# Kernel tuning notes

Measured on AMD Instinct MI355X. Metric: run time of the kernel, lower is better.

## Reference

```python
import jax, jax.numpy as jnp
import numpy as np

HIDDEN = 2048
NUM_HEADS = 16
HEAD_DIM = HIDDEN // NUM_HEADS


def setup_inputs() -> dict:
    key = jax.random.key(0)
    ks = jax.random.split(key, 5)
    B, S, H = 2, 2048, HIDDEN
    # xavier_uniform bounds
    qkv_bound = float(np.sqrt(6.0 / (H + 3 * H)))
    out_bound = float(np.sqrt(6.0 / (H + H)))
    return {
        "x": jax.random.normal(ks[0], (B, S, H), dtype=jnp.float32),
        "W_qkv": jax.random.uniform(ks[1], (3 * H, H), minval=-qkv_bound, maxval=qkv_bound, dtype=jnp.float32),
        "b_qkv": jnp.zeros((3 * H,), dtype=jnp.float32),
        "W_out": jax.random.uniform(ks[2], (H, H), minval=-out_bound, maxval=out_bound, dtype=jnp.float32),
        "b_out": jnp.zeros((H,), dtype=jnp.float32),
    }


def reference(x, W_qkv, b_qkv, W_out, b_out):
    B, S, H = x.shape
    # fused QKV projection (torch Linear: x @ W.T + b)
    qkv = x @ W_qkv.T + b_qkv                      # (B, S, 3H)
    q, k, v = jnp.split(qkv, 3, axis=-1)
    # (B, S, H) -> (B, N, S, D)
    def to_heads(t):
        return t.reshape(B, S, NUM_HEADS, HEAD_DIM).transpose(0, 2, 1, 3)
    q, k, v = to_heads(q), to_heads(k), to_heads(v)
    scale = HEAD_DIM ** -0.5
    scores = jnp.einsum("bnqd,bnkd->bnqk", q, k) * scale  # (B, N, S, S)
    causal = jnp.triu(jnp.ones((S, S), dtype=bool), k=1)
    scores = jnp.where(causal, -jnp.inf, scores)
    attn = jax.nn.softmax(scores, axis=-1)
    out = jnp.einsum("bnqk,bnkd->bnqd", attn, v)           # (B, N, S, D)
    out = out.transpose(0, 2, 1, 3).reshape(B, S, H)
    return out @ W_out.T + b_out
```

## Files before the change

kernel.cpp:

```cpp
#include <hip/hip_runtime.h>
#include <stdint.h>


using bf16x8 = __attribute__((ext_vector_type(8))) __bf16;
using f32x4  = __attribute__((ext_vector_type(4))) float;

#define S_LEN 2048
#define HID   2048
#define NHEAD 16
#define DHEAD 128
#define QSCALE_L2E (0.08838834764831845f * 1.4426950408889634f)

__device__ __forceinline__ unsigned short f2bf(float f) {
  union { float f; unsigned int u; } c; c.f = f;
  unsigned int u = c.u;
  return (unsigned short)((u + 0x7FFFu + ((u >> 16) & 1u)) >> 16);
}

__device__ __forceinline__ unsigned int pkbf(float a, float b) {
  union { __bf16 h[2]; unsigned int u; } x;
  x.h[0] = (__bf16)a; x.h[1] = (__bf16)b;
  return x.u;
}

__device__ __forceinline__ void gload_lds16(const void* g, void* l) {
  __builtin_amdgcn_global_load_lds(
      (const __attribute__((address_space(1))) unsigned int*)g,
      (__attribute__((address_space(3))) unsigned int*)l, 16, 0, 0);
}

__device__ __forceinline__ f32x4 mfma16(bf16x8 a, bf16x8 b, f32x4 c) {
  return __builtin_amdgcn_mfma_f32_16x16x32_bf16(a, b, c, 0, 0, 0);
}

__device__ __forceinline__ float hmax4(f32x4 v) {
  return fmaxf(fmaxf(v[0], v[1]), fmaxf(v[2], v[3]));
}

__global__ void cvt_bf16(const float* __restrict__ in, unsigned short* __restrict__ out, int n) {
  const int n4 = n >> 2;
  const int stride = gridDim.x * blockDim.x;
  for (int i = blockIdx.x * blockDim.x + threadIdx.x; i < n4; i += stride) {
    float4 v = reinterpret_cast<const float4*>(in)[i];
    ushort4 o;
    o.x = f2bf(v.x); o.y = f2bf(v.y); o.z = f2bf(v.z); o.w = f2bf(v.w);
    reinterpret_cast<ushort4*>(out)[i] = o;
  }
}

template<int EPI>
__global__ __launch_bounds__(256) void gemm_bt(
    const unsigned short* __restrict__ A, const unsigned short* __restrict__ Bw,
    const float* __restrict__ bias, int K, int N,
    unsigned short* __restrict__ q_out, unsigned short* __restrict__ k_out,
    unsigned short* __restrict__ vt_out, float* __restrict__ c_out)
{
  __shared__ char lsA[128 * 128];
  __shared__ char lsB[128 * 128];
  const int tid = threadIdx.x;
  const int l = tid & 63, w = tid >> 6;
  const int wr = w >> 1, wc = w & 1;
  const int bm = blockIdx.x * 128, bn = blockIdx.y * 128;
  const int row16 = l & 15, kg = l >> 4;

  f32x4 acc[4][4] = {};

  for (int k0 = 0; k0 < K; k0 += 64) {
    #pragma unroll
    for (int c = 0; c < 4; ++c) {
      const int o = c * 4096 + tid * 16;
      const int r = o >> 7;
      const int cb = (o & 127) ^ ((r & 7) << 4);
      gload_lds16((const char*)A + ((size_t)(bm + r) * K + k0) * 2 + cb,
                  lsA + c * 4096 + (w << 10));
      gload_lds16((const char*)Bw + ((size_t)(bn + r) * K + k0) * 2 + cb,
                  lsB + c * 4096 + (w << 10));
    }
    __syncthreads();

    #pragma unroll
    for (int h = 0; h < 2; ++h) {
      bf16x8 af[4], bfr[4];
      #pragma unroll
      for (int i = 0; i < 4; ++i) {
        const int ra = wr * 64 + i * 16 + row16;
        af[i]  = *(const bf16x8*)(lsA + ra * 128 + ((h * 64 + kg * 16) ^ ((ra & 7) << 4)));
        const int rb = wc * 64 + i * 16 + row16;
        bfr[i] = *(const bf16x8*)(lsB + rb * 128 + ((h * 64 + kg * 16) ^ ((rb & 7) << 4)));
      }
      #pragma unroll
      for (int i = 0; i < 4; ++i)
        #pragma unroll
        for (int j = 0; j < 4; ++j)
          acc[i][j] = mfma16(af[i], bfr[j], acc[i][j]);
    }
    __syncthreads();
  }

  const int r0 = kg * 4;
  #pragma unroll
  for (int i = 0; i < 4; ++i) {
    const int row = bm + wr * 64 + i * 16 + r0;
    #pragma unroll
    for (int j = 0; j < 4; ++j) {
      const int col = bn + wc * 64 + j * 16 + row16;
      const float bv = bias[col];
      if (EPI == 1) {
        #pragma unroll
        for (int r = 0; r < 4; ++r)
          c_out[(size_t)(row + r) * N + col] = acc[i][j][r] + bv;
      } else {
        const int sec = col >> 11;
        const int within = col & 2047;
        const int head = within >> 7, d = within & 127;
        #pragma unroll
        for (int r = 0; r < 4; ++r) {
          const int rr = row + r;
          const int b = rr >> 11, s = rr & 2047;
          const int bh = b * NHEAD + head;
          const float v = acc[i][j][r] + bv;
          if (sec == 0)
            q_out[((size_t)bh * S_LEN + s) * DHEAD + d] = f2bf(v * QSCALE_L2E);
          else if (sec == 1)
            k_out[((size_t)bh * S_LEN + s) * DHEAD + d] = f2bf(v);
          else
            vt_out[((size_t)bh * DHEAD + d) * S_LEN + s] = f2bf(v);
        }
      }
    }
  }
}

__global__ __launch_bounds__(256, 2) void attn_fwd(
    const unsigned short* __restrict__ Q, const unsigned short* __restrict__ Kk,
    const unsigned short* __restrict__ Vt, unsigned short* __restrict__ O)
{
  __shared__ char lsK[2][64 * 256];
  __shared__ char lsV[2][128 * 128];
  __shared__ char lsP[4][32 * 128];
  const int tid = threadIdx.x, l = tid & 63, w = tid >> 6;
  const int row16 = l & 15, kg = l >> 4;
  const int qb = (blockIdx.y < 16) ? (15 - (int)blockIdx.x) : (int)blockIdx.x;
  const int bh = blockIdx.y;
  const int bidx = bh >> 4, head = bh & 15;

  const char* Qh = (const char*)(Q  + (size_t)bh * S_LEN * DHEAD);
  const char* Kh = (const char*)(Kk + (size_t)bh * S_LEN * DHEAD);
  const char* Vh = (const char*)(Vt + (size_t)bh * DHEAD * S_LEN);

  const int q0w = qb * 128 + w * 32;

  bf16x8 qf[2][4];
  #pragma unroll
  for (int qs = 0; qs < 2; ++qs)
    #pragma unroll
    for (int t = 0; t < 4; ++t)
      qf[qs][t] = *(const bf16x8*)(Qh + ((size_t)(q0w + qs * 16 + row16) * DHEAD + t * 32 + kg * 8) * 2);

  float m[2]  = {-1e30f, -1e30f};
  float ls[2] = {0.f, 0.f};
  f32x4 oacc[2][8] = {};

  const int last = 2 * qb + 1;

#define STAGE(buf, kt_) do {                                                     \
    _Pragma("unroll")                                                            \
    for (int c = 0; c < 4; ++c) {                                                \
      const int o = c * 4096 + tid * 16;                                         \
      const int rk = o >> 8, cbk = (o & 255) ^ ((rk & 7) << 4);                  \
      gload_lds16(Kh + (size_t)((kt_) * 64 + rk) * 256 + cbk,                    \
                  lsK[buf] + c * 4096 + (w << 10));                              \
      const int dv = o >> 7, cbv = (o & 127) ^ ((dv & 7) << 4);                  \
      gload_lds16(Vh + (size_t)dv * 4096 + (size_t)(kt_) * 128 + cbv,            \
                  lsV[buf] + c * 4096 + (w << 10));                              \
    } } while (0)

  STAGE(0, 0);
  __syncthreads();

  int cur = 0;
  for (int kt = 0; ; ++kt) {
    if (kt < last) STAGE(cur ^ 1, kt + 1);

    if (kt * 64 <= q0w + 31) {
      const char* Kc = lsK[cur];
      const char* Vc = lsV[cur];
      char* Pl = lsP[w];

      f32x4 sc[4][2] = {};
      #pragma unroll
      for (int j = 0; j < 4; ++j) {
        const int krow = j * 16 + row16;
        const int sw = (krow & 7) << 4;
        bf16x8 kf[4];
        #pragma unroll
        for (int t = 0; t < 4; ++t)
          kf[t] = *(const bf16x8*)(Kc + krow * 256 + ((t * 64 + kg * 16) ^ sw));
        #pragma unroll
        for (int t = 0; t < 4; ++t) {
          sc[j][0] = mfma16(kf[t], qf[0][t], sc[j][0]);
          sc[j][1] = mfma16(kf[t], qf[1][t], sc[j][1]);
        }
      }

      if (kt >= 2 * qb) {
        #pragma unroll
        for (int j = 0; j < 4; ++j) {
          const int kvb = kt * 64 + j * 16 + kg * 4;
          #pragma unroll
          for (int qs = 0; qs < 2; ++qs) {
            const int qq = q0w + qs * 16 + row16;
            #pragma unroll
            for (int r = 0; r < 4; ++r)
              if (kvb + r > qq) sc[j][qs][r] = -1e30f;
          }
        }
      }

      float pm[2], al[2] = {1.f, 1.f};
      #pragma unroll
      for (int qs = 0; qs < 2; ++qs) {
        float mx = fmaxf(fmaxf(hmax4(sc[0][qs]), hmax4(sc[1][qs])),
                         fmaxf(hmax4(sc[2][qs]), hmax4(sc[3][qs])));
        mx = fmaxf(mx, __shfl_xor(mx, 16, 64));
        mx = fmaxf(mx, __shfl_xor(mx, 32, 64));
        pm[qs] = mx;
      }
      const bool need = (pm[0] > m[0] + 8.f) || (pm[1] > m[1] + 8.f);
      if (__any(need)) {
        const float n0 = fmaxf(m[0], pm[0]), n1 = fmaxf(m[1], pm[1]);
        al[0] = exp2f(m[0] - n0); al[1] = exp2f(m[1] - n1);
        m[0] = n0; m[1] = n1;
        float aq[2][4];
        #pragma unroll
        for (int qs2 = 0; qs2 < 2; ++qs2)
          #pragma unroll
          for (int r = 0; r < 4; ++r)
            aq[qs2][r] = __shfl(al[qs2], kg * 4 + r, 64);
        #pragma unroll
        for (int qs2 = 0; qs2 < 2; ++qs2)
          #pragma unroll
          for (int dt = 0; dt < 8; ++dt)
            #pragma unroll
            for (int r = 0; r < 4; ++r)
              oacc[qs2][dt][r] *= aq[qs2][r];
      }

      #pragma unroll
      for (int qs = 0; qs < 2; ++qs) {
        const int q = qs * 16 + row16;
        const int psw = (q & 7) << 4;
        float ps = 0.f;
        #pragma unroll
        for (int j = 0; j < 4; ++j) {
          const float p0 = exp2f(sc[j][qs][0] - m[qs]);
          const float p1 = exp2f(sc[j][qs][1] - m[qs]);
          const float p2 = exp2f(sc[j][qs][2] - m[qs]);
          const float p3 = exp2f(sc[j][qs][3] - m[qs]);
          ps += (p0 + p1) + (p2 + p3);
          uint2 pw; pw.x = pkbf(p0, p1); pw.y = pkbf(p2, p3);
          *(uint2*)(Pl + q * 128 + ((j * 32 + kg * 8) ^ psw)) = pw;
        }
        ps += __shfl_xor(ps, 16, 64);
        ps += __shfl_xor(ps, 32, 64);
        ls[qs] = ls[qs] * al[qs] + ps;
      }

      bf16x8 pa[2][2];
      #pragma unroll
      for (int qs2 = 0; qs2 < 2; ++qs2) {
        const int q = qs2 * 16 + row16;
        #pragma unroll
        for (int ks = 0; ks < 2; ++ks)
          pa[qs2][ks] = *(const bf16x8*)(Pl + q * 128 + ((ks * 64 + kg * 16) ^ ((q & 7) << 4)));
      }
      #pragma unroll
      for (int dt = 0; dt < 8; ++dt) {
        const int drow = dt * 16 + row16;
        const int vsw = (drow & 7) << 4;
        bf16x8 v0 = *(const bf16x8*)(Vc + drow * 128 + ((kg * 16) ^ vsw));
        bf16x8 v1 = *(const bf16x8*)(Vc + drow * 128 + ((64 + kg * 16) ^ vsw));
        oacc[0][dt] = mfma16(pa[0][0], v0, oacc[0][dt]);
        oacc[0][dt] = mfma16(pa[0][1], v1, oacc[0][dt]);
        oacc[1][dt] = mfma16(pa[1][0], v0, oacc[1][dt]);
        oacc[1][dt] = mfma16(pa[1][1], v1, oacc[1][dt]);
      }
    }

    __syncthreads();
    if (kt == last) break;
    cur ^= 1;
  }
#undef STAGE

  #pragma unroll
  for (int qs2 = 0; qs2 < 2; ++qs2) {
    #pragma unroll
    for (int r = 0; r < 4; ++r) {
      const float lr = __shfl(ls[qs2], kg * 4 + r, 64);
      const float inv = 1.0f / lr;
      const int q = q0w + qs2 * 16 + kg * 4 + r;
      const size_t orow = (size_t)(bidx * S_LEN + q) * HID + (size_t)head * DHEAD;
      #pragma unroll
      for (int dt = 0; dt < 8; ++dt)
        O[orow + dt * 16 + row16] = f2bf(oacc[qs2][dt][r] * inv);
    }
  }
}

extern "C" void kernel_launch(void* const* d_in, const int* in_sizes, int n_in,
                              void* d_out, int out_size, void* d_ws, size_t ws_size,
                              hipStream_t stream) {
  const float* x    = (const float*)d_in[0];
  const float* Wqkv = (const float*)d_in[1];
  const float* bqkv = (const float*)d_in[2];
  const float* Wout = (const float*)d_in[3];
  const float* bout = (const float*)d_in[4];
  float* out = (float*)d_out;

  if (ws_size < 100663296) return;
  char* ws = (char*)d_ws;
  unsigned short* Qb    = (unsigned short*)(ws);
  unsigned short* Kb    = (unsigned short*)(ws + 16777216);
  unsigned short* Vtb   = (unsigned short*)(ws + 2 * 16777216);
  unsigned short* xb    = (unsigned short*)(ws + 3 * 16777216);
  unsigned short* Ob    = xb;
  unsigned short* Wqkvb = (unsigned short*)(ws + 4 * 16777216);
  unsigned short* Woutb = (unsigned short*)(ws + 4 * 16777216 + 25165824);

  cvt_bf16<<<2048, 256, 0, stream>>>(x,    xb,    4096 * 2048);
  cvt_bf16<<<2048, 256, 0, stream>>>(Wqkv, Wqkvb, 6144 * 2048);
  cvt_bf16<<<1024, 256, 0, stream>>>(Wout, Woutb, 2048 * 2048);

  gemm_bt<0><<<dim3(32, 48), 256, 0, stream>>>(xb, Wqkvb, bqkv, 2048, 6144,
                                               Qb, Kb, Vtb, nullptr);
  attn_fwd<<<dim3(16, 32), 256, 0, stream>>>(Qb, Kb, Vtb, Ob);
  gemm_bt<1><<<dim3(32, 16), 256, 0, stream>>>(Ob, Woutb, bout, 2048, 2048,
                                               nullptr, nullptr, nullptr, out);
}
```

Measured before the change: 284.3 us.

## Replace GEMM with triple-buffered 512-thread kernel using larger tiles and block swizzle

The old 128x128 single-buffered GEMM kernel is replaced with a templated kernel that uses 256x256 or 128x256 tiles and 512 threads. It keeps a three-slot LDS ring of K=32 chunks, issuing async global-to-LDS loads two chunks ahead and waiting with explicit vmcnt counters. It also adds a blockIdx swizzle for L2 locality, a different LDS swizzle layout, and s_setprio around the MFMA block. The aim is to overlap memory loads with MFMA work and raise data reuse per tile, at the cost of more LDS and registers per block and reliance on hand-tuned waitcnt correctness.

```diff
diff --git a/kernel.cpp b/kernel.cpp
--- a/kernel.cpp
+++ b/kernel.cpp
@@ -9,6 +9,7 @@
 #define HID   2048
 #define NHEAD 16
 #define DHEAD 128
+#define KDIM  2048
 #define QSCALE_L2E (0.08838834764831845f * 1.4426950408889634f)
 
 __device__ __forceinline__ unsigned short f2bf(float f) {
@@ -35,6 +36,12 @@
 
 __device__ __forceinline__ float hmax4(f32x4 v) {
   return fmaxf(fmaxf(v[0], v[1]), fmaxf(v[2], v[3]));
+}
+
+template<int N> __device__ __forceinline__ void waitvm() {
+  if constexpr (N == 3)      asm volatile("s_waitcnt vmcnt(3)" ::: "memory");
+  else if constexpr (N == 4) asm volatile("s_waitcnt vmcnt(4)" ::: "memory");
+  else                       asm volatile("s_waitcnt vmcnt(0)" ::: "memory");
 }
 
 __global__ void cvt_bf16(const float* __restrict__ in, unsigned short* __restrict__ out, int n) {
@@ -48,62 +55,117 @@
   }
 }
 
-template<int EPI>
-__global__ __launch_bounds__(256) void gemm_bt(
+template<int BM, int BN, int EPI>
+__global__ __launch_bounds__(512, 2) void gemm_p3(
     const unsigned short* __restrict__ A, const unsigned short* __restrict__ Bw,
-    const float* __restrict__ bias, int K, int N,
+    const float* __restrict__ bias, int N,
     unsigned short* __restrict__ q_out, unsigned short* __restrict__ k_out,
     unsigned short* __restrict__ vt_out, float* __restrict__ c_out)
 {
-  __shared__ char lsA[128 * 128];
-  __shared__ char lsB[128 * 128];
-  const int tid = threadIdx.x;
-  const int l = tid & 63, w = tid >> 6;
-  const int wr = w >> 1, wc = w & 1;
-  const int bm = blockIdx.x * 128, bn = blockIdx.y * 128;
+  constexpr int KB2   = 2 * KDIM;
+  constexpr int NCH   = KDIM / 32;
+  constexpr int ABYT  = BM * 64;
+  constexpr int BBYT  = BN * 64;
+  constexpr int LPA   = BM / 128;
+  constexpr int LPB   = BN / 128;
+  constexpr int LPC   = LPA + LPB;
+  constexpr int M_SUB = BM / 32;
+  constexpr int N_SUB = BN / 64;
+  constexpr int MBC   = 4096 / BM;
+
+  __shared__ char lsA[3 * ABYT];
+  __shared__ char lsB[3 * BBYT];
+
+  const int tid = threadIdx.x, l = tid & 63, w = tid >> 6;
+  const int wr = w >> 2, wc = w & 3;
   const int row16 = l & 15, kg = l >> 4;
 
-  f32x4 acc[4][4] = {};
-
-  for (int k0 = 0; k0 < K; k0 += 64) {
-    #pragma unroll
-    for (int c = 0; c < 4; ++c) {
-      const int o = c * 4096 + tid * 16;
-      const int r = o >> 7;
-      const int cb = (o & 127) ^ ((r & 7) << 4);
-      gload_lds16((const char*)A + ((size_t)(bm + r) * K + k0) * 2 + cb,
-                  lsA + c * 4096 + (w << 10));
-      gload_lds16((const char*)Bw + ((size_t)(bn + r) * K + k0) * 2 + cb,
-                  lsB + c * 4096 + (w << 10));
+  const int nwg = gridDim.x;
+  const int bid = blockIdx.x;
+  const int swz = (bid & 7) * (nwg >> 3) + (bid >> 3);
+  const int bm = (swz % MBC) * BM, bn = (swz / MBC) * BN;
+
+  const char* Ag = (const char*)A + (size_t)bm * KB2;
+  const char* Bg = (const char*)Bw + (size_t)bn * KB2;
+
+  f32x4 acc[M_SUB][N_SUB] = {};
+
+#define STAGE(cc, sl) do {                                                     \
+    _Pragma("unroll")                                                          \
+    for (int p = 0; p < LPA; ++p) {                                            \
+      const int ob = (p * 8 + w) << 10;                                        \
+      const int o = ob + l * 16;                                               \
+      const int m2 = o >> 7, sw = o & 127;                                     \
+      const int t = sw ^ (((m2 << 1) & 7) << 4);                               \
+      const int odd = (t >> 6) & 1;                                            \
+      const int m = (m2 << 1) | odd;                                           \
+      const int kb = (t ^ (odd << 4)) & 63;                                    \
+      gload_lds16(Ag + (size_t)m * KB2 + (cc) * 64 + kb,                       \
+                  lsA + (sl) * ABYT + ob);                                     \
+    }                                                                          \
+    _Pragma("unroll")                                                          \
+    for (int p = 0; p < LPB; ++p) {                                            \
+      const int ob = (p * 8 + w) << 10;                                        \
+      const int o = ob + l * 16;                                               \
+      const int m2 = o >> 7, sw = o & 127;                                     \
+      const int t = sw ^ (((m2 << 1) & 7) << 4);                               \
+      const int odd = (t >> 6) & 1;                                            \
+      const int m = (m2 << 1) | odd;                                           \
+      const int kb = (t ^ (odd << 4)) & 63;                                    \
+      gload_lds16(Bg + (size_t)m * KB2 + (cc) * 64 + kb,                       \
+                  lsB + (sl) * BBYT + ob);                                     \
+    } } while (0)
+
+  STAGE(0, 0);
+  STAGE(1, 1);
+  waitvm<LPC>();
+  asm volatile("s_barrier" ::: "memory");
+
+  int sl = 0;
+  for (int c = 0; c < NCH; ++c) {
+    int cs = c + 2; if (cs >= NCH) cs -= NCH;
+    int s2 = sl + 2; if (s2 >= 3) s2 -= 3;
+    STAGE(cs, s2);
+
+    const char* Ac = lsA + sl * ABYT;
+    const char* Bc = lsB + sl * BBYT;
+    bf16x8 af[M_SUB], bf[N_SUB];
+    #pragma unroll
+    for (int i = 0; i < M_SUB; ++i) {
+      const int m = wr * (BM / 2) + i * 16 + row16;
+      af[i] = *(const bf16x8*)(Ac + (m >> 1) * 128 +
+              ((((m & 1) << 6) | (kg << 4)) ^ ((m & 7) << 4)));
     }
-    __syncthreads();
-
-    #pragma unroll
-    for (int h = 0; h < 2; ++h) {
-      bf16x8 af[4], bfr[4];
-      #pragma unroll
-      for (int i = 0; i < 4; ++i) {
-        const int ra = wr * 64 + i * 16 + row16;
-        af[i]  = *(const bf16x8*)(lsA + ra * 128 + ((h * 64 + kg * 16) ^ ((ra & 7) << 4)));
-        const int rb = wc * 64 + i * 16 + row16;
-        bfr[i] = *(const bf16x8*)(lsB + rb * 128 + ((h * 64 + kg * 16) ^ ((rb & 7) << 4)));
-      }
-      #pragma unroll
-      for (int i = 0; i < 4; ++i)
-        #pragma unroll
-        for (int j = 0; j < 4; ++j)
-          acc[i][j] = mfma16(af[i], bfr[j], acc[i][j]);
+    #pragma unroll
+    for (int j = 0; j < N_SUB; ++j) {
+      const int n = wc * (BN / 4) + j * 16 + row16;
+      bf[j] = *(const bf16x8*)(Bc + (n >> 1) * 128 +
+              ((((n & 1) << 6) | (kg << 4)) ^ ((n & 7) << 4)));
     }
-    __syncthreads();
+
+    __builtin_amdgcn_s_setprio(1);
+    #pragma unroll
+    for (int i = 0; i < M_SUB; ++i)
+      #pragma unroll
+      for (int j = 0; j < N_SUB; ++j)
+        acc[i][j] = mfma16(af[i], bf[j], acc[i][j]);
+    __builtin_amdgcn_s_setprio(0);
+
+    waitvm<LPC>();
+    __builtin_amdgcn_sched_barrier(0);
+    asm volatile("s_barrier" ::: "memory");
+
+    sl = sl + 1; if (sl == 3) sl = 0;
   }
-
-  const int r0 = kg * 4;
+#undef STAGE
+  waitvm<0>();
+
   #pragma unroll
-  for (int i = 0; i < 4; ++i) {
-    const int row = bm + wr * 64 + i * 16 + r0;
-    #pragma unroll
-    for (int j = 0; j < 4; ++j) {
-      const int col = bn + wc * 64 + j * 16 + row16;
+  for (int i = 0; i < M_SUB; ++i) {
+    const int row = bm + wr * (BM / 2) + i * 16 + kg * 4;
+    #pragma unroll
+    for (int j = 0; j < N_SUB; ++j) {
+      const int col = bn + wc * (BN / 4) + j * 16 + row16;
       const float bv = bias[col];
       if (EPI == 1) {
         #pragma unroll
@@ -332,9 +394,9 @@
   cvt_bf16<<<2048, 256, 0, stream>>>(Wqkv, Wqkvb, 6144 * 2048);
   cvt_bf16<<<1024, 256, 0, stream>>>(Wout, Woutb, 2048 * 2048);
 
-  gemm_bt<0><<<dim3(32, 48), 256, 0, stream>>>(xb, Wqkvb, bqkv, 2048, 6144,
-                                               Qb, Kb, Vtb, nullptr);
+  gemm_p3<256, 256, 0><<<384, 512, 0, stream>>>(xb, Wqkvb, bqkv, 6144,
+                                                Qb, Kb, Vtb, nullptr);
   attn_fwd<<<dim3(16, 32), 256, 0, stream>>>(Qb, Kb, Vtb, Ob);
-  gemm_bt<1><<<dim3(32, 16), 256, 0, stream>>>(Ob, Woutb, bout, 2048, 2048,
-                                               nullptr, nullptr, nullptr, out);
-}
+  gemm_p3<128, 256, 1><<<256, 512, 0, stream>>>(Ob, Woutb, bout, 2048,
+                                                nullptr, nullptr, nullptr, out);
+}
```

Result: slower. 385.8 us (+35.7%).

## Replace QKV GEMM with 256x256-tile, 8-wave, double-buffered pipelined kernel

Applied to the files above, without the earlier changes.

Swaps the QKV projection GEMM for a dedicated kernel using 256x256 output tiles, 512 threads and double-buffered LDS. Global-to-LDS loads for the next K chunk are interleaved with MFMA phases using explicit barriers, waitcnts and setprio, and block IDs are swizzled for L2 reuse. This aims to hide memory latency and raise data reuse per tile. The cost is 128KB of LDS per block and fragile hand-written synchronisation; the output GEMM is split out as its own non-templated kernel with the same behaviour.

```diff
diff --git a/kernel.cpp b/kernel.cpp
--- a/kernel.cpp
+++ b/kernel.cpp
@@ -9,6 +9,7 @@
 #define HID   2048
 #define NHEAD 16
 #define DHEAD 128
+#define KDIM  2048
 #define QSCALE_L2E (0.08838834764831845f * 1.4426950408889634f)
 
 __device__ __forceinline__ unsigned short f2bf(float f) {
@@ -48,13 +49,169 @@
   }
 }
 
-template<int EPI>
-__global__ __launch_bounds__(256) void gemm_bt(
+__global__ __launch_bounds__(512, 2) void gemm_qkv8(
     const unsigned short* __restrict__ A, const unsigned short* __restrict__ Bw,
-    const float* __restrict__ bias, int K, int N,
+    const float* __restrict__ bias,
     unsigned short* __restrict__ q_out, unsigned short* __restrict__ k_out,
-    unsigned short* __restrict__ vt_out, float* __restrict__ c_out)
+    unsigned short* __restrict__ vt_out)
 {
+  __shared__ char lsA[2][32768];
+  __shared__ char lsB[2][32768];
+  const int tid = threadIdx.x, l = tid & 63, w = tid >> 6;
+  const int wr = w >> 2, wc = w & 3;
+  const int row16 = l & 15, kg = l >> 4;
+
+  const int bid = blockIdx.x;
+  const int swz = (bid & 7) * 48 + (bid >> 3);
+  const int bm = (swz & 15) * 256, bn = (swz >> 4) * 256;
+  const char* Ag = (const char*)A + (size_t)bm * (KDIM * 2);
+  const char* Bg = (const char*)Bw + (size_t)bn * (KDIM * 2);
+
+  f32x4 acc[8][4] = {};
+
+  float bv[4];
+  #pragma unroll
+  for (int j = 0; j < 4; ++j) bv[j] = bias[bn + wc * 64 + j * 16 + row16];
+  asm volatile("" :: "v"(bv[0]), "v"(bv[1]), "v"(bv[2]), "v"(bv[3]));
+
+#define BAR   asm volatile("s_barrier" ::: "memory")
+#define LGKM0 asm volatile("s_waitcnt lgkmcnt(0)" ::: "memory"); __builtin_amdgcn_sched_barrier(0)
+#define VM4   asm volatile("s_waitcnt vmcnt(4)" ::: "memory")
+#define PRIO1 __builtin_amdgcn_s_setprio(1)
+#define PRIO0 __builtin_amdgcn_s_setprio(0)
+
+#define STAGE_A(buf, k0, qa) do {                                              \
+    _Pragma("unroll")                                                          \
+    for (int p = 0; p < 2; ++p) {                                              \
+      const int o = tid * 16;                                                  \
+      const int r = p * 128 + (qa) * 64 + (o >> 7);                            \
+      const int cb = (o & 127) ^ ((r & 7) << 4);                               \
+      gload_lds16(Ag + (size_t)r * (KDIM * 2) + (k0) * 2 + cb,                 \
+                  lsA[buf] + p * 16384 + (qa) * 8192 + o);                     \
+    } } while (0)
+
+#define STAGE_B(buf, k0, qb) do {                                              \
+    _Pragma("unroll")                                                          \
+    for (int p = 0; p < 2; ++p) {                                              \
+      const int o = tid * 16;                                                  \
+      const int blk = o >> 12;                                                 \
+      const int r = p * 128 + blk * 64 + (qb) * 32 + ((o >> 7) & 31);          \
+      const int cb = (o & 127) ^ ((r & 7) << 4);                               \
+      gload_lds16(Bg + (size_t)r * (KDIM * 2) + (k0) * 2 + cb,                 \
+                  lsB[buf] + p * 16384 + blk * 8192 + (qb) * 4096 + (o & 4095)); \
+    } } while (0)
+
+#define RD_A(dst, i0) do { _Pragma("unroll")                                   \
+    for (int i = 0; i < 4; ++i) {                                              \
+      const int m = wr * 128 + ((i0) + i) * 16 + row16;                        \
+      _Pragma("unroll")                                                        \
+      for (int h = 0; h < 2; ++h)                                              \
+        dst[i][h] = *(const bf16x8*)(Ac + m * 128 + ((h * 64 + kg * 16) ^ ((m & 7) << 4))); \
+    } } while (0)
+
+#define RD_B(dst, j0) do { _Pragma("unroll")                                   \
+    for (int j = 0; j < 2; ++j) {                                              \
+      const int n = wc * 64 + ((j0) + j) * 16 + row16;                         \
+      _Pragma("unroll")                                                        \
+      for (int h = 0; h < 2; ++h)                                              \
+        dst[j][h] = *(const bf16x8*)(Bc + n * 128 + ((h * 64 + kg * 16) ^ ((n & 7) << 4))); \
+    } } while (0)
+
+#define MM(afrag, bfrag, i0, j0) do { _Pragma("unroll")                        \
+    for (int i = 0; i < 4; ++i) { _Pragma("unroll")                            \
+      for (int j = 0; j < 2; ++j) { _Pragma("unroll")                          \
+        for (int h = 0; h < 2; ++h)                                            \
+          acc[(i0) + i][(j0) + j] = mfma16(afrag[i][h], bfrag[j][h], acc[(i0) + i][(j0) + j]); \
+    } } } while (0)
+
+  STAGE_A(0, 0, 0); STAGE_B(0, 0, 0); STAGE_A(0, 0, 1); STAGE_B(0, 0, 1);
+  asm volatile("s_waitcnt vmcnt(0)" ::: "memory");
+  BAR;
+
+  bf16x8 afl[4][2], afh[4][2], bfl[2][2], bfh[2][2];
+  constexpr int NCH = KDIM / 64;
+
+  #pragma unroll 1
+  for (int t = 0; t < NCH - 1; ++t) {
+    const int cur = t & 1, nxt = cur ^ 1;
+    const char* Ac = lsA[cur];
+    const char* Bc = lsB[cur];
+    const int k1 = (t + 1) * 64;
+    RD_A(afl, 0); RD_B(bfl, 0);
+    STAGE_A(nxt, k1, 0);
+    BAR; LGKM0;
+    PRIO1; MM(afl, bfl, 0, 0); PRIO0;
+    VM4; BAR;
+    RD_A(afh, 4);
+    STAGE_B(nxt, k1, 0);
+    BAR; LGKM0;
+    PRIO1; MM(afh, bfl, 4, 0); PRIO0;
+    VM4; BAR;
+    RD_B(bfh, 2);
+    STAGE_A(nxt, k1, 1);
+    BAR; LGKM0;
+    PRIO1; MM(afl, bfh, 0, 2); PRIO0;
+    BAR;
+    STAGE_B(nxt, k1, 1);
+    BAR;
+    PRIO1; MM(afh, bfh, 4, 2); PRIO0;
+    VM4; BAR;
+  }
+  {
+    const char* Ac = lsA[(NCH - 1) & 1];
+    const char* Bc = lsB[(NCH - 1) & 1];
+    RD_A(afl, 0); RD_B(bfl, 0);
+    MM(afl, bfl, 0, 0);
+    asm volatile("s_waitcnt vmcnt(2)" ::: "memory");
+    RD_A(afh, 4);
+    MM(afh, bfl, 4, 0);
+    asm volatile("s_waitcnt vmcnt(0)" ::: "memory");
+    RD_B(bfh, 2);
+    MM(afl, bfh, 0, 2);
+    MM(afh, bfh, 4, 2);
+  }
+#undef STAGE_A
+#undef STAGE_B
+#undef RD_A
+#undef RD_B
+#undef MM
+#undef BAR
+#undef LGKM0
+#undef VM4
+#undef PRIO1
+#undef PRIO0
+
+  #pragma unroll
+  for (int i = 0; i < 8; ++i) {
+    const int row = bm + wr * 128 + i * 16 + kg * 4;
+    #pragma unroll
+    for (int j = 0; j < 4; ++j) {
+      const int col = bn + wc * 64 + j * 16 + row16;
+      const int sec = col >> 11;
+      const int within = col & 2047;
+      const int head = within >> 7, d = within & 127;
+      #pragma unroll
+      for (int r = 0; r < 4; ++r) {
+        const int rr = row + r;
+        const int b = rr >> 11, s = rr & 2047;
+        const int bh = b * NHEAD + head;
+        const float v = acc[i][j][r] + bv[j];
+        if (sec == 0)
+          q_out[((size_t)bh * S_LEN + s) * DHEAD + d] = f2bf(v * QSCALE_L2E);
+        else if (sec == 1)
+          k_out[((size_t)bh * S_LEN + s) * DHEAD + d] = f2bf(v);
+        else
+          vt_out[((size_t)bh * DHEAD + d) * S_LEN + s] = f2bf(v);
+      }
+    }
+  }
+}
+
+__global__ __launch_bounds__(256) void gemm_out(
+    const unsigned short* __restrict__ A, const unsigned short* __restrict__ Bw,
+    const float* __restrict__ bias, float* __restrict__ c_out)
+{
+  constexpr int K = KDIM, N = HID;
   __shared__ char lsA[128 * 128];
   __shared__ char lsB[128 * 128];
   const int tid = threadIdx.x;
@@ -97,36 +254,16 @@
     __syncthreads();
   }
 
-  const int r0 = kg * 4;
   #pragma unroll
   for (int i = 0; i < 4; ++i) {
-    const int row = bm + wr * 64 + i * 16 + r0;
+    const int row = bm + wr * 64 + i * 16 + kg * 4;
     #pragma unroll
     for (int j = 0; j < 4; ++j) {
       const int col = bn + wc * 64 + j * 16 + row16;
-      const float bv = bias[col];
-      if (EPI == 1) {
-        #pragma unroll
-        for (int r = 0; r < 4; ++r)
-          c_out[(size_t)(row + r) * N + col] = acc[i][j][r] + bv;
-      } else {
-        const int sec = col >> 11;
-        const int within = col & 2047;
-        const int head = within >> 7, d = within & 127;
-        #pragma unroll
-        for (int r = 0; r < 4; ++r) {
-          const int rr = row + r;
-          const int b = rr >> 11, s = rr & 2047;
-          const int bh = b * NHEAD + head;
-          const float v = acc[i][j][r] + bv;
-          if (sec == 0)
-            q_out[((size_t)bh * S_LEN + s) * DHEAD + d] = f2bf(v * QSCALE_L2E);
-          else if (sec == 1)
-            k_out[((size_t)bh * S_LEN + s) * DHEAD + d] = f2bf(v);
-          else
-            vt_out[((size_t)bh * DHEAD + d) * S_LEN + s] = f2bf(v);
-        }
-      }
+      const float bvj = bias[col];
+      #pragma unroll
+      for (int r = 0; r < 4; ++r)
+        c_out[(size_t)(row + r) * N + col] = acc[i][j][r] + bvj;
     }
   }
 }
@@ -332,9 +469,7 @@
   cvt_bf16<<<2048, 256, 0, stream>>>(Wqkv, Wqkvb, 6144 * 2048);
   cvt_bf16<<<1024, 256, 0, stream>>>(Wout, Woutb, 2048 * 2048);
 
-  gemm_bt<0><<<dim3(32, 48), 256, 0, stream>>>(xb, Wqkvb, bqkv, 2048, 6144,
-                                               Qb, Kb, Vtb, nullptr);
+  gemm_qkv8<<<384, 512, 0, stream>>>(xb, Wqkvb, bqkv, Qb, Kb, Vtb);
   attn_fwd<<<dim3(16, 32), 256, 0, stream>>>(Qb, Kb, Vtb, Ob);
-  gemm_bt<1><<<dim3(32, 16), 256, 0, stream>>>(Ob, Woutb, bout, 2048, 2048,
-                                               nullptr, nullptr, nullptr, out);
-}
+  gemm_out<<<dim3(32, 16), 256, 0, stream>>>(Ob, Woutb, bout, out);
+}
```

New measurement: 317.4 us. 11.6% more time.

## Replace generic GEMM with multi-stage pipelined 512-thread QKV and output GEMMs

Applied to the files above, without the earlier changes.

Splits the templated GEMM into two specialized kernels. The QKV GEMM uses 256x384 tiles with a 3-stage LDS ring, and the output GEMM uses 128x256 tiles with a 4-stage ring. Both use 512 threads, K-step 64, explicit vmcnt waits, raw s_barrier and MFMA priority boosting, and a swizzled block order for L2 reuse. The aim is to overlap global loads with MFMA work and cut per-iteration sync overhead, at the cost of larger LDS use, more registers and a single wave of 256 blocks with hardcoded sizes.

```diff
diff --git a/kernel.cpp b/kernel.cpp
--- a/kernel.cpp
+++ b/kernel.cpp
@@ -9,6 +9,7 @@
 #define HID   2048
 #define NHEAD 16
 #define DHEAD 128
+#define KDIM  2048
 #define QSCALE_L2E (0.08838834764831845f * 1.4426950408889634f)
 
 __device__ __forceinline__ unsigned short f2bf(float f) {
@@ -48,85 +49,225 @@
   }
 }
 
-template<int EPI>
-__global__ __launch_bounds__(256) void gemm_bt(
+#define BAR   asm volatile("s_barrier" ::: "memory")
+#define VM(n) asm volatile("s_waitcnt vmcnt(" #n ")" ::: "memory")
+#define PRIO1 __builtin_amdgcn_s_setprio(1)
+#define PRIO0 __builtin_amdgcn_s_setprio(0)
+
+
+__global__ __launch_bounds__(512) void gemm_qkv(
     const unsigned short* __restrict__ A, const unsigned short* __restrict__ Bw,
-    const float* __restrict__ bias, int K, int N,
+    const float* __restrict__ bias,
     unsigned short* __restrict__ q_out, unsigned short* __restrict__ k_out,
-    unsigned short* __restrict__ vt_out, float* __restrict__ c_out)
+    unsigned short* __restrict__ vt_out)
 {
-  __shared__ char lsA[128 * 128];
-  __shared__ char lsB[128 * 128];
-  const int tid = threadIdx.x;
-  const int l = tid & 63, w = tid >> 6;
-  const int wr = w >> 1, wc = w & 1;
-  const int bm = blockIdx.x * 128, bn = blockIdx.y * 128;
+  constexpr int ABYT = 256 * 64;
+  constexpr int BBYT = 384 * 64;
+  __shared__ char lsA[3 * ABYT];
+  __shared__ char lsB[3 * BBYT];
+
+  const int tid = threadIdx.x, l = tid & 63, w = tid >> 6;
+  const int wr = w >> 2, wc = w & 3;
   const int row16 = l & 15, kg = l >> 4;
 
+  const int bid = blockIdx.x;
+  const int swz = (bid & 7) * 32 + (bid >> 3);
+  const int bm = (swz & 15) * 256, bn = (swz >> 4) * 384;
+  const char* Ag = (const char*)A + (size_t)bm * (KDIM * 2);
+  const char* Bg = (const char*)Bw + (size_t)bn * (KDIM * 2);
+
+  f32x4 acc[8][6] = {};
+
+#define STAGE_A(cc, dstb) do { _Pragma("unroll")                               \
+    for (int p = 0; p < 2; ++p) {                                              \
+      const int o = p * 8192 + tid * 16;                                       \
+      const int r = o >> 6, c = o & 63;                                        \
+      gload_lds16(Ag + (size_t)r * (KDIM * 2) + (cc) * 64 +                    \
+                  (c ^ (((r >> 1) & 3) << 4)),                                 \
+                  (dstb) + p * 8192 + (w << 10));                              \
+    } } while (0)
+
+#define STAGE_B(cc, dstb) do { _Pragma("unroll")                               \
+    for (int p = 0; p < 3; ++p) {                                              \
+      const int o = p * 8192 + tid * 16;                                       \
+      const int r = o >> 6, c = o & 63;                                        \
+      gload_lds16(Bg + (size_t)r * (KDIM * 2) + (cc) * 64 +                    \
+                  (c ^ (((r >> 1) & 3) << 4)),                                 \
+                  (dstb) + p * 8192 + (w << 10));                              \
+    } } while (0)
+
+  STAGE_A(0, lsA); STAGE_B(0, lsB);
+  STAGE_A(1, lsA + ABYT); STAGE_B(1, lsB + BBYT);
+  VM(5);
+  BAR;
+
+  int sl = 0;
+  #pragma unroll 1
+  for (int t = 0; t < 64; ++t) {
+    const int s2 = (sl == 0) ? 2 : sl - 1;
+    const char* Ac = lsA + sl * ABYT;
+    const char* Bc = lsB + sl * BBYT;
+    char* A2 = lsA + s2 * ABYT;
+    char* B2 = lsB + s2 * BBYT;
+
+    bf16x8 af[8], bl[3], bh[3];
+    if (t < 62) STAGE_A(t + 2, A2);
+    #pragma unroll
+    for (int i = 0; i < 8; ++i) {
+      const int m = wr * 128 + i * 16 + row16;
+      af[i] = *(const bf16x8*)(Ac + m * 64 + ((kg * 16) ^ (((m >> 1) & 3) << 4)));
+    }
+    #pragma unroll
+    for (int j = 0; j < 3; ++j) {
+      const int n = wc * 96 + j * 16 + row16;
+      bl[j] = *(const bf16x8*)(Bc + n * 64 + ((kg * 16) ^ (((n >> 1) & 3) << 4)));
+    }
+    PRIO1;
+    #pragma unroll
+    for (int i = 0; i < 8; ++i)
+      #pragma unroll
+      for (int j = 0; j < 3; ++j)
+        acc[i][j] = mfma16(af[i], bl[j], acc[i][j]);
+    PRIO0;
+    BAR;
+
+    if (t < 62) STAGE_B(t + 2, B2);
+    #pragma unroll
+    for (int j = 0; j < 3; ++j) {
+      const int n = wc * 96 + (j + 3) * 16 + row16;
+      bh[j] = *(const bf16x8*)(Bc + n * 64 + ((kg * 16) ^ (((n >> 1) & 3) << 4)));
+    }
+    PRIO1;
+    #pragma unroll
+    for (int i = 0; i < 8; ++i)
+      #pragma unroll
+      for (int j = 0; j < 3; ++j)
+        acc[i][j + 3] = mfma16(af[i], bh[j], acc[i][j + 3]);
+    PRIO0;
+    if (t < 62)      VM(5);
+    else if (t == 62) VM(0);
+    BAR;
+
+    sl = (sl == 2) ? 0 : sl + 1;
+  }
+#undef STAGE_A
+#undef STAGE_B
+
+  #pragma unroll
+  for (int j = 0; j < 6; ++j) {
+    const int col = bn + wc * 96 + j * 16 + row16;
+    const float bvj = bias[col];
+    const int sec = col >> 11;
+    const int within = col & 2047;
+    const int head = within >> 7, d = within & 127;
+    #pragma unroll
+    for (int i = 0; i < 8; ++i) {
+      const int row = bm + wr * 128 + i * 16 + kg * 4;
+      #pragma unroll
+      for (int r = 0; r < 4; ++r) {
+        const int rr = row + r;
+        const int b = rr >> 11, s = rr & 2047;
+        const int bh2 = b * NHEAD + head;
+        const float v = acc[i][j][r] + bvj;
+        if (sec == 0)
+          q_out[((size_t)bh2 * S_LEN + s) * DHEAD + d] = f2bf(v * QSCALE_L2E);
+        else if (sec == 1)
+          k_out[((size_t)bh2 * S_LEN + s) * DHEAD + d] = f2bf(v);
+        else
+          vt_out[((size_t)bh2 * DHEAD + d) * S_LEN + s] = f2bf(v);
+      }
+    }
+  }
+}
+
+__global__ __launch_bounds__(512) void gemm_out(
+    const unsigned short* __restrict__ A, const unsigned short* __restrict__ Bw,
+    const float* __restrict__ bias, float* __restrict__ c_out)
+{
+  constexpr int ABYT = 128 * 64;
+  constexpr int BBYT = 256 * 64;
+  __shared__ char lsA[4 * ABYT];
+  __shared__ char lsB[4 * BBYT];
+
+  const int tid = threadIdx.x, l = tid & 63, w = tid >> 6;
+  const int wr = w >> 2, wc = w & 3;
+  const int row16 = l & 15, kg = l >> 4;
+
+  const int bid = blockIdx.x;
+  const int swz = (bid & 7) * 32 + (bid >> 3);
+  const int bm = (swz & 31) * 128, bn = (swz >> 5) * 256;
+  const char* Ag = (const char*)A + (size_t)bm * (KDIM * 2);
+  const char* Bg = (const char*)Bw + (size_t)bn * (KDIM * 2);
+
   f32x4 acc[4][4] = {};
 
-  for (int k0 = 0; k0 < K; k0 += 64) {
-    #pragma unroll
-    for (int c = 0; c < 4; ++c) {
-      const int o = c * 4096 + tid * 16;
-      const int r = o >> 7;
-      const int cb = (o & 127) ^ ((r & 7) << 4);
-      gload_lds16((const char*)A + ((size_t)(bm + r) * K + k0) * 2 + cb,
-                  lsA + c * 4096 + (w << 10));
-      gload_lds16((const char*)Bw + ((size_t)(bn + r) * K + k0) * 2 + cb,
-                  lsB + c * 4096 + (w << 10));
-    }
-    __syncthreads();
-
-    #pragma unroll
-    for (int h = 0; h < 2; ++h) {
-      bf16x8 af[4], bfr[4];
-      #pragma unroll
-      for (int i = 0; i < 4; ++i) {
-        const int ra = wr * 64 + i * 16 + row16;
-        af[i]  = *(const bf16x8*)(lsA + ra * 128 + ((h * 64 + kg * 16) ^ ((ra & 7) << 4)));
-        const int rb = wc * 64 + i * 16 + row16;
-        bfr[i] = *(const bf16x8*)(lsB + rb * 128 + ((h * 64 + kg * 16) ^ ((rb & 7) << 4)));
-      }
-      #pragma unroll
-      for (int i = 0; i < 4; ++i)
-        #pragma unroll
-        for (int j = 0; j < 4; ++j)
-          acc[i][j] = mfma16(af[i], bfr[j], acc[i][j]);
-    }
-    __syncthreads();
-  }
-
-  const int r0 = kg * 4;
+#define STAGE_A(cc, dstb) do {                                                 \
+    const int o = tid * 16;                                                    \
+    const int r = o >> 6, c = o & 63;                                          \
+    gload_lds16(Ag + (size_t)r * (KDIM * 2) + (cc) * 64 +                      \
+                (c ^ (((r >> 1) & 3) << 4)),                                   \
+                (dstb) + (w << 10));                                           \
+  } while (0)
+
+#define STAGE_B(cc, dstb) do { _Pragma("unroll")                               \
+    for (int p = 0; p < 2; ++p) {                                              \
+      const int o = p * 8192 + tid * 16;                                       \
+      const int r = o >> 6, c = o & 63;                                        \
+      gload_lds16(Bg + (size_t)r * (KDIM * 2) + (cc) * 64 +                    \
+                  (c ^ (((r >> 1) & 3) << 4)),                                 \
+                  (dstb) + p * 8192 + (w << 10));                              \
+    } } while (0)
+
+  STAGE_A(0, lsA);              STAGE_B(0, lsB);
+  STAGE_A(1, lsA + ABYT);       STAGE_B(1, lsB + BBYT);
+  STAGE_A(2, lsA + 2 * ABYT);   STAGE_B(2, lsB + 2 * BBYT);
+  VM(6);
+  BAR;
+
+  #pragma unroll 1
+  for (int t = 0; t < 64; ++t) {
+    const int sl = t & 3, s3 = (t + 3) & 3;
+    const char* Ac = lsA + sl * ABYT;
+    const char* Bc = lsB + sl * BBYT;
+
+    if (t < 61) { STAGE_A(t + 3, lsA + s3 * ABYT); STAGE_B(t + 3, lsB + s3 * BBYT); }
+
+    bf16x8 af[4], bf[4];
+    #pragma unroll
+    for (int i = 0; i < 4; ++i) {
+      const int m = wr * 64 + i * 16 + row16;
+      af[i] = *(const bf16x8*)(Ac + m * 64 + ((kg * 16) ^ (((m >> 1) & 3) << 4)));
+    }
+    #pragma unroll
+    for (int j = 0; j < 4; ++j) {
+      const int n = wc * 64 + j * 16 + row16;
+      bf[j] = *(const bf16x8*)(Bc + n * 64 + ((kg * 16) ^ (((n >> 1) & 3) << 4)));
+    }
+    PRIO1;
+    #pragma unroll
+    for (int i = 0; i < 4; ++i)
+      #pragma unroll
+      for (int j = 0; j < 4; ++j)
+        acc[i][j] = mfma16(af[i], bf[j], acc[i][j]);
+    PRIO0;
+    if (t < 61)       VM(6);
+    else if (t == 61) VM(3);
+    else if (t == 62) VM(0);
+    BAR;
+  }
+#undef STAGE_A
+#undef STAGE_B
+
   #pragma unroll
   for (int i = 0; i < 4; ++i) {
-    const int row = bm + wr * 64 + i * 16 + r0;
+    const int row = bm + wr * 64 + i * 16 + kg * 4;
     #pragma unroll
     for (int j = 0; j < 4; ++j) {
       const int col = bn + wc * 64 + j * 16 + row16;
-      const float bv = bias[col];
-      if (EPI == 1) {
-        #pragma unroll
-        for (int r = 0; r < 4; ++r)
-          c_out[(size_t)(row + r) * N + col] = acc[i][j][r] + bv;
-      } else {
-        const int sec = col >> 11;
-        const int within = col & 2047;
-        const int head = within >> 7, d = within & 127;
-        #pragma unroll
-        for (int r = 0; r < 4; ++r) {
-          const int rr = row + r;
-          const int b = rr >> 11, s = rr & 2047;
-          const int bh = b * NHEAD + head;
-          const float v = acc[i][j][r] + bv;
-          if (sec == 0)
-            q_out[((size_t)bh * S_LEN + s) * DHEAD + d] = f2bf(v * QSCALE_L2E);
-          else if (sec == 1)
-            k_out[((size_t)bh * S_LEN + s) * DHEAD + d] = f2bf(v);
-          else
-            vt_out[((size_t)bh * DHEAD + d) * S_LEN + s] = f2bf(v);
-        }
-      }
+      const float bvj = bias[col];
+      #pragma unroll
+      for (int r = 0; r < 4; ++r)
+        c_out[(size_t)(row + r) * HID + col] = acc[i][j][r] + bvj;
     }
   }
 }
@@ -332,9 +473,7 @@
   cvt_bf16<<<2048, 256, 0, stream>>>(Wqkv, Wqkvb, 6144 * 2048);
   cvt_bf16<<<1024, 256, 0, stream>>>(Wout, Woutb, 2048 * 2048);
 
-  gemm_bt<0><<<dim3(32, 48), 256, 0, stream>>>(xb, Wqkvb, bqkv, 2048, 6144,
-                                               Qb, Kb, Vtb, nullptr);
+  gemm_qkv<<<256, 512, 0, stream>>>(xb, Wqkvb, bqkv, Qb, Kb, Vtb);
   attn_fwd<<<dim3(16, 32), 256, 0, stream>>>(Qb, Kb, Vtb, Ob);
-  gemm_bt<1><<<dim3(32, 16), 256, 0, stream>>>(Ob, Woutb, bout, 2048, 2048,
-                                               nullptr, nullptr, nullptr, out);
-}
+  gemm_out<<<256, 512, 0, stream>>>(Ob, Woutb, bout, out);
+}
```

After: 319.4 us. 1.12x slower.
